# Optimization experiments

Measured on AMD Instinct MI355X. Metric: run time of the kernel, lower is better.

Reference implementation:

```python
import jax, jax.numpy as jnp
import numpy as np

T, H, N, D = 4096, 16, 16, 64


def setup_inputs() -> dict:
    key = jax.random.key(0)
    ks = jax.random.split(key, 8)
    x = jax.random.normal(ks[0], (T, H, D), dtype=jnp.float32)
    dt = jax.random.uniform(ks[1], (T, H), dtype=jnp.float32) * 0.1  # small positive timesteps
    B = jax.random.normal(ks[2], (T, H, N), dtype=jnp.float32)
    C = jax.random.normal(ks[3], (T, H, N), dtype=jnp.float32)
    mask = jax.random.randint(ks[4], (T,), 0, 2).astype(jnp.float32)  # reset flags in {0,1}
    initial_carry = jax.random.normal(ks[5], (H, N, D), dtype=jnp.float32)
    log_decay = jax.random.normal(ks[6], (H,), dtype=jnp.float32) * 0.1
    skip_weight = jnp.ones((H, D), dtype=jnp.float32)
    return {"x": x, "dt": dt, "B": B, "C": C, "mask": mask,
            "initial_carry": initial_carry, "log_decay": log_decay,
            "skip_weight": skip_weight}


def _binary_operator(q_i, q_j):
    # elementwise; broadcasting replaces the original per-time vmap
    a_i, b_i, c_i = q_i
    a_j, b_j, c_j = q_j
    a_out = a_j * a_i * (1.0 - c_j) + a_j * c_j
    b_out = (a_j * b_i + b_j) * (1.0 - c_j) + b_j * c_j
    c_out = c_i * (1.0 - c_j) + c_j
    return (a_out, b_out, c_out)


def reference(x, dt, B, C, mask, initial_carry, log_decay, skip_weight):
    num_heads = dt.shape[1]
    decay_rate = -jnp.exp(log_decay)                        # [H]
    decay_factor = jnp.exp(dt * decay_rate[None, :])        # [T,H]
    decay_factor = decay_factor[:, :, None, None]           # [T,H,1,1]
    decay_factor = jnp.concatenate(
        [jnp.ones((1, num_heads, 1, 1), dtype=decay_factor.dtype), decay_factor], axis=0)
    driving_input = jnp.einsum('th,thn,thd->thnd', dt, B, x)  # [T,H,N,D]
    driving_input = jnp.concatenate([initial_carry[None, ...], driving_input], axis=0)
    m = jnp.concatenate([jnp.zeros((1,), dtype=mask.dtype), mask])
    m = m[:, None, None, None]                              # [T+1,1,1,1]
    _, hidden_states, _ = jax.lax.associative_scan(
        _binary_operator, (decay_factor, driving_input, m))
    next_carry = hidden_states[-1]                          # [H,N,D]
    valid_states = hidden_states[1:]                        # [T,H,N,D]
    output = jnp.einsum('thn,thnd->thd', C, valid_states)   # [T,H,D]
    output = output + skip_weight[None, :, :] * x
    return (next_carry, output)
```

## Files before the change

### kernel.cpp

```cpp
#include <hip/hip_runtime.h>

#define T_LEN 4096
#define H 16
#define N 16
#define D 64
#define NC 128
#define CL (T_LEN / NC)


__global__ __launch_bounds__(64)
void phase1(const float* __restrict__ x, const float* __restrict__ dt,
            const float* __restrict__ B, const float* __restrict__ mask,
            const float* __restrict__ log_decay,
            float* __restrict__ Lbuf, float* __restrict__ Pbuf) {
    const int c = blockIdx.x, h = blockIdx.y;
    const int d = threadIdx.x;
    const float rate = -__expf(log_decay[h]);
    const int t0 = c * CL;

    __shared__ float Bs[CL * N];
    {
        const float4* Bg = (const float4*)B;
        float4* Bsv = (float4*)Bs;
#pragma unroll
        for (int i = 0; i < (CL * N / 4) / 64; ++i) {
            const int j = i * 64 + d;
            const int row = j >> 2, off = j & 3;
            const float dtv = dt[(t0 + row) * H + h];
            float4 bv = Bg[((t0 + row) * H + h) * (N / 4) + off];
            bv.x *= dtv; bv.y *= dtv; bv.z *= dtv; bv.w *= dtv;
            Bsv[j] = bv;
        }
    }
    __syncthreads();

    float s[N];
#pragma unroll
    for (int n = 0; n < N; ++n) s[n] = 0.f;
    float P = 1.f;

#pragma unroll
    for (int ss = 0; ss < CL; ++ss) {
        const int t = t0 + ss;
        const float dtv = dt[t * H + h];
        const float mv  = mask[t];
        const float a   = (1.f - mv) * __expf(dtv * rate);
        const float xv  = x[(t * H + h) * D + d];
        P *= a;
        const float4* Br4 = (const float4*)(Bs + ss * N);
#pragma unroll
        for (int q = 0; q < 4; ++q) {
            const float4 bv = Br4[q];
            s[4*q+0] = a * s[4*q+0] + bv.x * xv;
            s[4*q+1] = a * s[4*q+1] + bv.y * xv;
            s[4*q+2] = a * s[4*q+2] + bv.z * xv;
            s[4*q+3] = a * s[4*q+3] + bv.w * xv;
        }
    }

    float* Lp = Lbuf + ((c * H + h) * N) * D + d;
#pragma unroll
    for (int n = 0; n < N; ++n)
        __builtin_nontemporal_store(s[n], Lp + n * D);
    if (d == 0) Pbuf[h * NC + c] = P;
}

__global__ __launch_bounds__(256)
void phase2(const float* __restrict__ initial_carry,
            float* __restrict__ LE, const float* __restrict__ Pbuf,
            float* __restrict__ next_carry) {
    const int idx = blockIdx.x * 256 + threadIdx.x;
    const int h = blockIdx.x >> 2;
    float carry = initial_carry[idx];

#pragma unroll
    for (int r = 0; r < NC / 64; ++r) {
        float l[64];
#pragma unroll
        for (int k = 0; k < 64; ++k)
            l[k] = LE[(r * 64 + k) * (H * N * D) + idx];
#pragma unroll
        for (int k = 0; k < 64; ++k) {
            const float p = Pbuf[h * NC + r * 64 + k];
            LE[(r * 64 + k) * (H * N * D) + idx] = carry;
            carry = p * carry + l[k];
        }
    }
    next_carry[idx] = carry;
}

__global__ __launch_bounds__(64)
void phase3(const float* __restrict__ x, const float* __restrict__ dt,
            const float* __restrict__ B, const float* __restrict__ C,
            const float* __restrict__ mask, const float* __restrict__ log_decay,
            const float* __restrict__ skip_weight,
            const float* __restrict__ Ebuf, float* __restrict__ out) {
    const int c = blockIdx.x, h = blockIdx.y;
    const int d = threadIdx.x;
    const float rate = -__expf(log_decay[h]);
    const int t0 = c * CL;

    __shared__ float Bs[CL * N], Cs[CL * N];
    {
        const float4* Bg = (const float4*)B;
        const float4* Cg = (const float4*)C;
        float4* Bsv = (float4*)Bs;
        float4* Csv = (float4*)Cs;
#pragma unroll
        for (int i = 0; i < (CL * N / 4) / 64; ++i) {
            const int j = i * 64 + d;
            const int row = j >> 2, off = j & 3;
            const float dtv = dt[(t0 + row) * H + h];
            float4 bv = Bg[((t0 + row) * H + h) * (N / 4) + off];
            bv.x *= dtv; bv.y *= dtv; bv.z *= dtv; bv.w *= dtv;
            Bsv[j] = bv;
            Csv[j] = Cg[((t0 + row) * H + h) * (N / 4) + off];
        }
    }
    __syncthreads();

    float s[N];
    const float* Ep = Ebuf + ((c * H + h) * N) * D + d;
#pragma unroll
    for (int n = 0; n < N; ++n) s[n] = Ep[n * D];

    const float sw = skip_weight[h * D + d];
#pragma unroll
    for (int ss = 0; ss < CL; ++ss) {
        const int t = t0 + ss;
        const float dtv = dt[t * H + h];
        const float mv  = mask[t];
        const float a   = (1.f - mv) * __expf(dtv * rate);
        const float xv  = x[(t * H + h) * D + d];
        float acc = sw * xv;
        const float4* Br4 = (const float4*)(Bs + ss * N);
        const float4* Cr4 = (const float4*)(Cs + ss * N);
#pragma unroll
        for (int q = 0; q < 4; ++q) {
            const float4 bv = Br4[q];
            const float4 cv = Cr4[q];
            s[4*q+0] = a * s[4*q+0] + bv.x * xv;  acc += cv.x * s[4*q+0];
            s[4*q+1] = a * s[4*q+1] + bv.y * xv;  acc += cv.y * s[4*q+1];
            s[4*q+2] = a * s[4*q+2] + bv.z * xv;  acc += cv.z * s[4*q+2];
            s[4*q+3] = a * s[4*q+3] + bv.w * xv;  acc += cv.w * s[4*q+3];
        }
        __builtin_nontemporal_store(acc, &out[(t * H + h) * D + d]);
    }
}

extern "C" void kernel_launch(void* const* d_in, const int* in_sizes, int n_in,
                              void* d_out, int out_size, void* d_ws, size_t ws_size,
                              hipStream_t stream) {
    const float* x    = (const float*)d_in[0];
    const float* dt   = (const float*)d_in[1];
    const float* B    = (const float*)d_in[2];
    const float* C    = (const float*)d_in[3];
    const float* mask = (const float*)d_in[4];
    const float* ic   = (const float*)d_in[5];
    const float* ld   = (const float*)d_in[6];
    const float* sw   = (const float*)d_in[7];
    float* out = (float*)d_out;

    float* Lbuf = (float*)d_ws;
    float* Pbuf = Lbuf + (size_t)NC * H * N * D;

    dim3 grid(NC, H), block(64);
    phase1<<<grid, block, 0, stream>>>(x, dt, B, mask, ld, Lbuf, Pbuf);
    phase2<<<dim3(H * N * D / 256), dim3(256), 0, stream>>>(ic, Lbuf, Pbuf, out);
    phase3<<<grid, block, 0, stream>>>(x, dt, B, C, mask, ld, sw, Lbuf, out + H * N * D);
}
```

Measured before the change: 41.09 us.

## Store chunk states in bf16 and halve chunk count with split inner loop

Intermediate per-chunk states and propagated carries are now stored as bf16 instead of fp32, halving workspace traffic between the three phases. The chunk count drops from 128 to 64, so there are fewer cross-chunk carries in phase2 and longer sequential scans in phases 1 and 3. Those scans are split into two halves with a non-unrolled outer loop to limit code size. The bf16 rounding of carried states adds precision error that compounds through the recurrence, and the halved grid (1024 wavefronts) lowers parallelism.

```diff
diff --git a/kernel.cpp b/kernel.cpp
--- a/kernel.cpp
+++ b/kernel.cpp
@@ -4,15 +4,25 @@
 #define H 16
 #define N 16
 #define D 64
-#define NC 128
+#define NC 64
 #define CL (T_LEN / NC)
+#define CH (CL / 2)
 
+static __device__ __forceinline__ unsigned short f2bf(float f) {
+    union { float f; unsigned u; } v; v.f = f;
+    unsigned r = (v.u + 0x7fffu + ((v.u >> 16) & 1u)) >> 16;
+    return (unsigned short)r;
+}
+static __device__ __forceinline__ float bf2f(unsigned short s) {
+    union { unsigned u; float f; } v; v.u = ((unsigned)s) << 16;
+    return v.f;
+}
 
 __global__ __launch_bounds__(64)
 void phase1(const float* __restrict__ x, const float* __restrict__ dt,
             const float* __restrict__ B, const float* __restrict__ mask,
             const float* __restrict__ log_decay,
-            float* __restrict__ Lbuf, float* __restrict__ Pbuf) {
+            unsigned short* __restrict__ Lb, float* __restrict__ Pbuf) {
     const int c = blockIdx.x, h = blockIdx.y;
     const int d = threadIdx.x;
     const float rate = -__expf(log_decay[h]);
@@ -39,52 +49,52 @@
     for (int n = 0; n < N; ++n) s[n] = 0.f;
     float P = 1.f;
 
+#pragma unroll 1
+    for (int half = 0; half < 2; ++half) {
 #pragma unroll
-    for (int ss = 0; ss < CL; ++ss) {
-        const int t = t0 + ss;
-        const float dtv = dt[t * H + h];
-        const float mv  = mask[t];
-        const float a   = (1.f - mv) * __expf(dtv * rate);
-        const float xv  = x[(t * H + h) * D + d];
-        P *= a;
-        const float4* Br4 = (const float4*)(Bs + ss * N);
+        for (int s2 = 0; s2 < CH; ++s2) {
+            const int ss = half * CH + s2;
+            const int t = t0 + ss;
+            const float dtv = dt[t * H + h];
+            const float mv  = mask[t];
+            const float a   = (1.f - mv) * __expf(dtv * rate);
+            const float xv  = x[(t * H + h) * D + d];
+            P *= a;
+            const float4* Br4 = (const float4*)(Bs + ss * N);
 #pragma unroll
-        for (int q = 0; q < 4; ++q) {
-            const float4 bv = Br4[q];
-            s[4*q+0] = a * s[4*q+0] + bv.x * xv;
-            s[4*q+1] = a * s[4*q+1] + bv.y * xv;
-            s[4*q+2] = a * s[4*q+2] + bv.z * xv;
-            s[4*q+3] = a * s[4*q+3] + bv.w * xv;
+            for (int q = 0; q < 4; ++q) {
+                const float4 bv = Br4[q];
+                s[4*q+0] = a * s[4*q+0] + bv.x * xv;
+                s[4*q+1] = a * s[4*q+1] + bv.y * xv;
+                s[4*q+2] = a * s[4*q+2] + bv.z * xv;
+                s[4*q+3] = a * s[4*q+3] + bv.w * xv;
+            }
         }
     }
 
-    float* Lp = Lbuf + ((c * H + h) * N) * D + d;
+    unsigned short* Lp = Lb + ((c * H + h) * N) * D + d;
 #pragma unroll
-    for (int n = 0; n < N; ++n)
-        __builtin_nontemporal_store(s[n], Lp + n * D);
+    for (int n = 0; n < N; ++n) Lp[n * D] = f2bf(s[n]);
     if (d == 0) Pbuf[h * NC + c] = P;
 }
 
 __global__ __launch_bounds__(256)
 void phase2(const float* __restrict__ initial_carry,
-            float* __restrict__ LE, const float* __restrict__ Pbuf,
+            unsigned short* __restrict__ LE, const float* __restrict__ Pbuf,
             float* __restrict__ next_carry) {
     const int idx = blockIdx.x * 256 + threadIdx.x;
     const int h = blockIdx.x >> 2;
     float carry = initial_carry[idx];
 
+    float l[NC];
 #pragma unroll
-    for (int r = 0; r < NC / 64; ++r) {
-        float l[64];
+    for (int k = 0; k < NC; ++k)
+        l[k] = bf2f(LE[k * (H * N * D) + idx]);
 #pragma unroll
-        for (int k = 0; k < 64; ++k)
-            l[k] = LE[(r * 64 + k) * (H * N * D) + idx];
-#pragma unroll
-        for (int k = 0; k < 64; ++k) {
-            const float p = Pbuf[h * NC + r * 64 + k];
-            LE[(r * 64 + k) * (H * N * D) + idx] = carry;
-            carry = p * carry + l[k];
-        }
+    for (int k = 0; k < NC; ++k) {
+        const float p = Pbuf[h * NC + k];
+        LE[k * (H * N * D) + idx] = f2bf(carry);
+        carry = p * carry + l[k];
     }
     next_carry[idx] = carry;
 }
@@ -94,7 +104,7 @@
             const float* __restrict__ B, const float* __restrict__ C,
             const float* __restrict__ mask, const float* __restrict__ log_decay,
             const float* __restrict__ skip_weight,
-            const float* __restrict__ Ebuf, float* __restrict__ out) {
+            const unsigned short* __restrict__ Eb, float* __restrict__ out) {
     const int c = blockIdx.x, h = blockIdx.y;
     const int d = threadIdx.x;
     const float rate = -__expf(log_decay[h]);
@@ -120,31 +130,35 @@
     __syncthreads();
 
     float s[N];
-    const float* Ep = Ebuf + ((c * H + h) * N) * D + d;
+    const unsigned short* Ep = Eb + ((c * H + h) * N) * D + d;
 #pragma unroll
-    for (int n = 0; n < N; ++n) s[n] = Ep[n * D];
+    for (int n = 0; n < N; ++n) s[n] = bf2f(Ep[n * D]);
 
     const float sw = skip_weight[h * D + d];
+#pragma unroll 1
+    for (int half = 0; half < 2; ++half) {
 #pragma unroll
-    for (int ss = 0; ss < CL; ++ss) {
-        const int t = t0 + ss;
-        const float dtv = dt[t * H + h];
-        const float mv  = mask[t];
-        const float a   = (1.f - mv) * __expf(dtv * rate);
-        const float xv  = x[(t * H + h) * D + d];
-        float acc = sw * xv;
-        const float4* Br4 = (const float4*)(Bs + ss * N);
-        const float4* Cr4 = (const float4*)(Cs + ss * N);
+        for (int s2 = 0; s2 < CH; ++s2) {
+            const int ss = half * CH + s2;
+            const int t = t0 + ss;
+            const float dtv = dt[t * H + h];
+            const float mv  = mask[t];
+            const float a   = (1.f - mv) * __expf(dtv * rate);
+            const float xv  = x[(t * H + h) * D + d];
+            float acc = sw * xv;
+            const float4* Br4 = (const float4*)(Bs + ss * N);
+            const float4* Cr4 = (const float4*)(Cs + ss * N);
 #pragma unroll
-        for (int q = 0; q < 4; ++q) {
-            const float4 bv = Br4[q];
-            const float4 cv = Cr4[q];
-            s[4*q+0] = a * s[4*q+0] + bv.x * xv;  acc += cv.x * s[4*q+0];
-            s[4*q+1] = a * s[4*q+1] + bv.y * xv;  acc += cv.y * s[4*q+1];
-            s[4*q+2] = a * s[4*q+2] + bv.z * xv;  acc += cv.z * s[4*q+2];
-            s[4*q+3] = a * s[4*q+3] + bv.w * xv;  acc += cv.w * s[4*q+3];
+            for (int q = 0; q < 4; ++q) {
+                const float4 bv = Br4[q];
+                const float4 cv = Cr4[q];
+                s[4*q+0] = a * s[4*q+0] + bv.x * xv;  acc += cv.x * s[4*q+0];
+                s[4*q+1] = a * s[4*q+1] + bv.y * xv;  acc += cv.y * s[4*q+1];
+                s[4*q+2] = a * s[4*q+2] + bv.z * xv;  acc += cv.z * s[4*q+2];
+                s[4*q+3] = a * s[4*q+3] + bv.w * xv;  acc += cv.w * s[4*q+3];
+            }
+            __builtin_nontemporal_store(acc, &out[(t * H + h) * D + d]);
         }
-        __builtin_nontemporal_store(acc, &out[(t * H + h) * D + d]);
     }
 }
 
@@ -161,11 +175,11 @@
     const float* sw   = (const float*)d_in[7];
     float* out = (float*)d_out;
 
-    float* Lbuf = (float*)d_ws;
-    float* Pbuf = Lbuf + (size_t)NC * H * N * D;
+    float* Pbuf = (float*)d_ws;
+    unsigned short* Lb = (unsigned short*)((char*)d_ws + 4096);
 
     dim3 grid(NC, H), block(64);
-    phase1<<<grid, block, 0, stream>>>(x, dt, B, mask, ld, Lbuf, Pbuf);
-    phase2<<<dim3(H * N * D / 256), dim3(256), 0, stream>>>(ic, Lbuf, Pbuf, out);
-    phase3<<<grid, block, 0, stream>>>(x, dt, B, C, mask, ld, sw, Lbuf, out + H * N * D);
+    phase1<<<grid, block, 0, stream>>>(x, dt, B, mask, ld, Lb, Pbuf);
+    phase2<<<dim3(H * N * D / 256), dim3(256), 0, stream>>>(ic, Lb, Pbuf, out);
+    phase3<<<grid, block, 0, stream>>>(x, dt, B, C, mask, ld, sw, Lb, out + H * N * D);
 }
```

Measured after the change: 46.29 us. 12.7% more time.
